# Optimization experiments

Hardware: AMD Instinct MI355X
Metric: run time of the kernel (lower is better)

Reference implementation:

```python
import jax, jax.numpy as jnp
import numpy as np

B, D, N, H = 1024, 512, 16, 512  # batch, latent, branches, hidden


def _lrelu(v):
    return jnp.where(v >= 0, v, 0.1 * v)  # LeakyReLU(0.1)


def setup_inputs() -> dict:
    key = jax.random.key(0)
    ks = jax.random.split(key, 9)
    s = 0.02
    return {
        "x": jax.random.normal(ks[0], (B, D, N), dtype=jnp.float32),
        "Ws1": jax.random.normal(ks[1], (D, D), dtype=jnp.float32) * s,
        "bs1": jnp.zeros((D,), dtype=jnp.float32),
        "Ws2": jax.random.normal(ks[2], (D, D), dtype=jnp.float32) * s,
        "bs2": jnp.zeros((D,), dtype=jnp.float32),
        # per-branch binary classifiers: Linear(D,H)+LeakyReLU+Linear(H,1)
        "Wc1": jax.random.normal(ks[3], (N, D, H), dtype=jnp.float32) * s,
        "bc1": jnp.zeros((N, H), dtype=jnp.float32),
        "Wc2": jax.random.normal(ks[4], (N, H), dtype=jnp.float32) * s,
        "bc2": jnp.zeros((N,), dtype=jnp.float32),
    }


def reference(x, Ws1, bs1, Ws2, bs2, Wc1, bc1, Wc2, bc2):
    # x: [B, D, N] -> per-branch tokens [B, N, D]
    xb = jnp.transpose(x, (0, 2, 1))
    # shared MLP applied to every branch slice (same weights)
    h = _lrelu(xb @ Ws1 + bs1)
    shared = _lrelu(h @ Ws2 + bs2)  # [B, N, D]
    # per-branch classifier on its own branch slice -> sigmoid probs
    h1 = _lrelu(jnp.einsum('bnd,ndh->bnh', shared, Wc1) + bc1)
    logits = jnp.einsum('bnh,nh->bn', h1, Wc2) + bc2  # [B, N]
    out = jax.nn.sigmoid(logits)[:, None, :]  # [B, 1, N]
    # full pass: concat branch slices along batch (branch-major), every
    # classifier applied to the full stack -> raw logits
    full_in = jnp.transpose(shared, (1, 0, 2)).reshape(N * B, D)  # [M, D]
    h2 = _lrelu(jnp.einsum('md,ndh->mnh', full_in, Wc1) + bc1)  # [M, N, H]
    full_logits = jnp.einsum('mnh,nh->mn', h2, Wc2) + bc2  # [M, N]
    full_out = full_logits[:, None, :]  # [N*B, 1, N]
    return (out, full_out)
```

## Files before the change

kernel.cpp:

```cpp
#include <hip/hip_runtime.h>
#include <hip/hip_bf16.h>
#include <stdint.h>

#define Bq 1024
#define Dq 512
#define Nq 16
#define Hq 512
#define Mq (Bq*Nq)

typedef short v8s __attribute__((ext_vector_type(8)));
typedef float v4f __attribute__((ext_vector_type(4)));
typedef int   v4i __attribute__((ext_vector_type(4)));

__device__ __forceinline__ unsigned short f2bf(float f) {
  union { float f; unsigned u; } v; v.f = f;
  return (unsigned short)((v.u + 0x7fffu + ((v.u >> 16) & 1u)) >> 16);
}

__global__ void k_transpose_x(const float* __restrict__ x, unsigned short* __restrict__ xb) {
  __shared__ float lds[Dq][Nq + 1];
  const int b = blockIdx.x;
  const float* xi = x + (size_t)b * Dq * Nq;
  const int t = threadIdx.x;
  for (int p = 0; p < (Dq*Nq)/256; ++p) {
    int i = t + p*256;
    lds[i >> 4][i & (Nq-1)] = xi[i];
  }
  __syncthreads();
  unsigned short* o = xb + (size_t)b * Nq * Dq;
  for (int p = 0; p < (Dq*Nq)/256; ++p) {
    int i = t + p*256;
    o[i] = f2bf(lds[i & (Dq-1)][i >> 9]);
  }
}

__global__ void k_transpose_w(const float* __restrict__ in, unsigned short* __restrict__ out,
                              int R, int C) {
  __shared__ float tile[32][33];
  const int z = blockIdx.z;
  in  += (size_t)z * R * C;
  out += (size_t)z * R * C;
  const int tx = threadIdx.x, ty = threadIdx.y;
  const int c0 = blockIdx.x * 32, r0 = blockIdx.y * 32;
#pragma unroll
  for (int j = 0; j < 4; ++j)
    tile[ty + j*8][tx] = in[(size_t)(r0 + ty + j*8) * C + c0 + tx];
  __syncthreads();
#pragma unroll
  for (int j = 0; j < 4; ++j) {
    int c = c0 + ty + j*8;
    int r = r0 + tx;
    out[(size_t)c * R + r] = f2bf(tile[tx][ty + j*8]);
  }
}

template<int MODE>
__global__ __launch_bounds__(256)
void k_gemm(const unsigned short* __restrict__ A,
            const unsigned short* __restrict__ Bt,
            const float* __restrict__ bias,
            void* __restrict__ out_,
            const float* __restrict__ w2,
            int permute) {
  constexpr int BM = 128, BN = 128, BK = 32, KD = 512;
  __shared__ __align__(16) unsigned short As[BM][BK + 8];
  __shared__ __align__(16) unsigned short Bs[BN][BK + 8];

  const int t = threadIdx.x;
  const int wave = t >> 6, lane = t & 63;
  const int wr = wave >> 1, wc = wave & 1;
  const int quad = lane >> 4, l16 = lane & 15;
  const int bm = blockIdx.x * BM, bn = blockIdx.y * BN;
  const int z = blockIdx.z;

  const unsigned short* Bz = Bt + (size_t)z * KD * 512;
  const float* biasz = bias + (size_t)z * 512;

  v4f acc[4][4] = {};

  for (int kt = 0; kt < KD / BK; ++kt) {
#pragma unroll
    for (int p = 0; p < 2; ++p) {
      int c = t + p * 256;
      int row = c >> 2, kc = (c & 3) * 8;
      *(v4i*)&As[row][kc] = *(const v4i*)&A [(size_t)(bm + row) * KD + kt*BK + kc];
      *(v4i*)&Bs[row][kc] = *(const v4i*)&Bz[(size_t)(bn + row) * KD + kt*BK + kc];
    }
    __syncthreads();
    v8s af[4], bf[4];
#pragma unroll
    for (int mi = 0; mi < 4; ++mi)
      af[mi] = *(const v8s*)&As[wr*64 + mi*16 + l16][quad*8];
#pragma unroll
    for (int ni = 0; ni < 4; ++ni)
      bf[ni] = *(const v8s*)&Bs[wc*64 + ni*16 + l16][quad*8];
#pragma unroll
    for (int mi = 0; mi < 4; ++mi)
#pragma unroll
      for (int ni = 0; ni < 4; ++ni)
        acc[mi][ni] = __builtin_amdgcn_mfma_f32_16x16x32_bf16(af[mi], bf[ni], acc[mi][ni], 0, 0, 0);
    __syncthreads();
  }

  if (MODE == 0) {
    unsigned short* O = (unsigned short*)out_;
#pragma unroll
    for (int mi = 0; mi < 4; ++mi) {
#pragma unroll
      for (int r = 0; r < 4; ++r) {
        int grow = bm + wr*64 + mi*16 + quad*4 + r;
        int orow = permute ? ((grow & 15) * Bq + (grow >> 4)) : grow;
#pragma unroll
        for (int ni = 0; ni < 4; ++ni) {
          int col = bn + wc*64 + ni*16 + l16;
          float v = acc[mi][ni][r] + biasz[col];
          v = v >= 0.f ? v : 0.1f * v;
          O[(size_t)orow * 512 + col] = f2bf(v);
        }
      }
    }
  } else {
    float* FL = (float*)out_;
    const float* w2z = w2 + (size_t)z * 512;
#pragma unroll
    for (int mi = 0; mi < 4; ++mi) {
#pragma unroll
      for (int r = 0; r < 4; ++r) {
        float s = 0.f;
#pragma unroll
        for (int ni = 0; ni < 4; ++ni) {
          int col = bn + wc*64 + ni*16 + l16;
          float v = acc[mi][ni][r] + biasz[col];
          v = v >= 0.f ? v : 0.1f * v;
          s += v * w2z[col];
        }
#pragma unroll
        for (int off = 1; off < 16; off <<= 1)
          s += __shfl_xor(s, off, 64);
        if (l16 == 0) {
          int grow = bm + wr*64 + mi*16 + quad*4 + r;
          atomicAdd(&FL[(size_t)grow * Nq + z], s);
        }
      }
    }
  }
}

__global__ void k_final(const float* __restrict__ fl, const float* __restrict__ bc2,
                        float* __restrict__ out) {
  int i = blockIdx.x * 256 + threadIdx.x;
  int m = i >> 4, n = i & 15;
  float v = fl[i] + bc2[n];
  out[Mq + i] = v;
  if (n == (m >> 10)) {
    int b = m & (Bq - 1);
    out[b * Nq + n] = 1.f / (1.f + __expf(-v));
  }
}

extern "C" void kernel_launch(void* const* d_in, const int* in_sizes, int n_in,
                              void* d_out, int out_size, void* d_ws, size_t ws_size,
                              hipStream_t stream) {
  (void)in_sizes; (void)n_in; (void)out_size; (void)ws_size;
  const float* x   = (const float*)d_in[0];
  const float* Ws1 = (const float*)d_in[1];
  const float* bs1 = (const float*)d_in[2];
  const float* Ws2 = (const float*)d_in[3];
  const float* bs2 = (const float*)d_in[4];
  const float* Wc1 = (const float*)d_in[5];
  const float* bc1 = (const float*)d_in[6];
  const float* Wc2 = (const float*)d_in[7];
  const float* bc2 = (const float*)d_in[8];

  char* ws = (char*)d_ws;
  unsigned short* Xb   = (unsigned short*)(ws);
  unsigned short* Hbuf = (unsigned short*)(ws + (size_t)16*1024*1024);
  unsigned short* Sm   = (unsigned short*)(ws + (size_t)32*1024*1024);
  unsigned short* Ws1t = (unsigned short*)(ws + (size_t)48*1024*1024);
  unsigned short* Ws2t = (unsigned short*)(ws + (size_t)48*1024*1024 + 512*1024);
  unsigned short* Wc1t = (unsigned short*)(ws + (size_t)49*1024*1024);
  float*          FL   = (float*)         (ws + (size_t)57*1024*1024);

  hipMemsetAsync(FL, 0, (size_t)Mq * Nq * sizeof(float), stream);

  k_transpose_x<<<Bq, 256, 0, stream>>>(x, Xb);
  dim3 tb(32, 8);
  k_transpose_w<<<dim3(16,16,1),  tb, 0, stream>>>(Ws1, Ws1t, 512, 512);
  k_transpose_w<<<dim3(16,16,1),  tb, 0, stream>>>(Ws2, Ws2t, 512, 512);
  k_transpose_w<<<dim3(16,16,16), tb, 0, stream>>>(Wc1, Wc1t, 512, 512);

  k_gemm<0><<<dim3(128,4,1), 256, 0, stream>>>(Xb,   Ws1t, bs1, Hbuf, nullptr, 0);
  k_gemm<0><<<dim3(128,4,1), 256, 0, stream>>>(Hbuf, Ws2t, bs2, Sm,   nullptr, 1);
  k_gemm<1><<<dim3(128,4,16), 256, 0, stream>>>(Sm, Wc1t, bc1, FL, Wc2, 0);

  k_final<<<(Mq*Nq)/256, 256, 0, stream>>>(FL, bc2, (float*)d_out);
}
```

Before: 351.7 us.

## Load GEMM tiles directly into LDS with XOR swizzle; merge weight transposes

The GEMM's global-to-shared tile loads now use global_load_lds (direct global-to-LDS DMA) instead of going through registers. The unpadded LDS layout uses an XOR swizzle on 16-byte column groups to avoid bank conflicts on the MFMA fragment reads. The three weight-transpose launches are also merged into a single launch indexed by blockIdx.z. The goal is to cut VGPR use and instruction overhead in the load path and to remove launch overhead. The risk is that the swizzle indexing must match the per-lane destination layout of the LDS DMA exactly.

```diff
diff --git a/kernel.cpp b/kernel.cpp
--- a/kernel.cpp
+++ b/kernel.cpp
@@ -11,6 +11,9 @@
 typedef short v8s __attribute__((ext_vector_type(8)));
 typedef float v4f __attribute__((ext_vector_type(4)));
 typedef int   v4i __attribute__((ext_vector_type(4)));
+
+typedef __attribute__((address_space(3))) unsigned int as3_u32;
+typedef __attribute__((address_space(1))) const unsigned int as1_u32;
 
 __device__ __forceinline__ unsigned short f2bf(float f) {
   union { float f; unsigned u; } v; v.f = f;
@@ -34,23 +37,28 @@
   }
 }
 
-__global__ void k_transpose_w(const float* __restrict__ in, unsigned short* __restrict__ out,
-                              int R, int C) {
+__global__ void k_transpose_w(const float* __restrict__ Ws1, const float* __restrict__ Ws2,
+                              const float* __restrict__ Wc1,
+                              unsigned short* __restrict__ Ws1t, unsigned short* __restrict__ Ws2t,
+                              unsigned short* __restrict__ Wc1t) {
   __shared__ float tile[32][33];
   const int z = blockIdx.z;
-  in  += (size_t)z * R * C;
-  out += (size_t)z * R * C;
+  const float* in;
+  unsigned short* out;
+  if (z == 0)      { in = Ws1; out = Ws1t; }
+  else if (z == 1) { in = Ws2; out = Ws2t; }
+  else             { in = Wc1 + (size_t)(z-2) * 512 * 512; out = Wc1t + (size_t)(z-2) * 512 * 512; }
   const int tx = threadIdx.x, ty = threadIdx.y;
   const int c0 = blockIdx.x * 32, r0 = blockIdx.y * 32;
 #pragma unroll
   for (int j = 0; j < 4; ++j)
-    tile[ty + j*8][tx] = in[(size_t)(r0 + ty + j*8) * C + c0 + tx];
+    tile[ty + j*8][tx] = in[(size_t)(r0 + ty + j*8) * 512 + c0 + tx];
   __syncthreads();
 #pragma unroll
   for (int j = 0; j < 4; ++j) {
     int c = c0 + ty + j*8;
     int r = r0 + tx;
-    out[(size_t)c * R + r] = f2bf(tile[tx][ty + j*8]);
+    out[(size_t)c * 512 + r] = f2bf(tile[tx][ty + j*8]);
   }
 }
 
@@ -63,8 +71,8 @@
             const float* __restrict__ w2,
             int permute) {
   constexpr int BM = 128, BN = 128, BK = 32, KD = 512;
-  __shared__ __align__(16) unsigned short As[BM][BK + 8];
-  __shared__ __align__(16) unsigned short Bs[BN][BK + 8];
+  __shared__ __align__(16) unsigned short As[BM][BK];
+  __shared__ __align__(16) unsigned short Bs[BN][BK];
 
   const int t = threadIdx.x;
   const int wave = t >> 6, lane = t & 63;
@@ -76,24 +84,35 @@
   const unsigned short* Bz = Bt + (size_t)z * KD * 512;
   const float* biasz = bias + (size_t)z * 512;
 
+  const int srow0 = wave * 32;
+  const int lrow = lane >> 2;
+  const int lslot = lane & 3;
+
   v4f acc[4][4] = {};
 
   for (int kt = 0; kt < KD / BK; ++kt) {
 #pragma unroll
     for (int p = 0; p < 2; ++p) {
-      int c = t + p * 256;
-      int row = c >> 2, kc = (c & 3) * 8;
-      *(v4i*)&As[row][kc] = *(const v4i*)&A [(size_t)(bm + row) * KD + kt*BK + kc];
-      *(v4i*)&Bs[row][kc] = *(const v4i*)&Bz[(size_t)(bn + row) * KD + kt*BK + kc];
+      int r0 = srow0 + p * 16;
+      int row = r0 + lrow;
+      int cg = lslot ^ ((row >> 1) & 3);
+      const unsigned short* ga = &A [(size_t)(bm + row) * KD + kt*BK + cg*8];
+      const unsigned short* gb = &Bz[(size_t)(bn + row) * KD + kt*BK + cg*8];
+      __builtin_amdgcn_global_load_lds((as1_u32*)ga, (as3_u32*)&As[r0][0], 16, 0, 0);
+      __builtin_amdgcn_global_load_lds((as1_u32*)gb, (as3_u32*)&Bs[r0][0], 16, 0, 0);
     }
     __syncthreads();
     v8s af[4], bf[4];
 #pragma unroll
-    for (int mi = 0; mi < 4; ++mi)
-      af[mi] = *(const v8s*)&As[wr*64 + mi*16 + l16][quad*8];
-#pragma unroll
-    for (int ni = 0; ni < 4; ++ni)
-      bf[ni] = *(const v8s*)&Bs[wc*64 + ni*16 + l16][quad*8];
+    for (int mi = 0; mi < 4; ++mi) {
+      int ra = wr*64 + mi*16 + l16;
+      af[mi] = *(const v8s*)&As[ra][(quad ^ ((ra >> 1) & 3)) * 8];
+    }
+#pragma unroll
+    for (int ni = 0; ni < 4; ++ni) {
+      int rb = wc*64 + ni*16 + l16;
+      bf[ni] = *(const v8s*)&Bs[rb][(quad ^ ((rb >> 1) & 3)) * 8];
+    }
 #pragma unroll
     for (int mi = 0; mi < 4; ++mi)
 #pragma unroll
@@ -184,10 +203,7 @@
   hipMemsetAsync(FL, 0, (size_t)Mq * Nq * sizeof(float), stream);
 
   k_transpose_x<<<Bq, 256, 0, stream>>>(x, Xb);
-  dim3 tb(32, 8);
-  k_transpose_w<<<dim3(16,16,1),  tb, 0, stream>>>(Ws1, Ws1t, 512, 512);
-  k_transpose_w<<<dim3(16,16,1),  tb, 0, stream>>>(Ws2, Ws2t, 512, 512);
-  k_transpose_w<<<dim3(16,16,16), tb, 0, stream>>>(Wc1, Wc1t, 512, 512);
+  k_transpose_w<<<dim3(16,16,18), dim3(32,8), 0, stream>>>(Ws1, Ws2, Wc1, Ws1t, Ws2t, Wc1t);
 
   k_gemm<0><<<dim3(128,4,1), 256, 0, stream>>>(Xb,   Ws1t, bs1, Hbuf, nullptr, 0);
   k_gemm<0><<<dim3(128,4,1), 256, 0, stream>>>(Hbuf, Ws2t, bs2, Sm,   nullptr, 1);
```

Result: faster. 334.9 us (-4.8%).
